# Performance work log

Measured on AMD Instinct MI355X. Metric: run time of the kernel, lower is better.

## Reference

```python
import math
import jax, jax.numpy as jnp
import numpy as np

# ---------------- static irrep configuration ----------------
RS_IN = [(16, 0, 0), (16, 1, 0)]
RS_OUT = [(16, 0, 0), (16, 1, 0)]


def selection_rule(l_in, p_in, l_out, p_out):
    return [l for l in range(abs(l_in - l_out), l_in + l_out + 1)
            if p_out == 0 or p_in * (-1) ** l == p_out]


# ---------------- real Wigner 3j (Clebsch-Gordan) ----------------

def _su2_cg(j1, j2, j3, m1, m2, m3):
    if m1 + m2 != m3:
        return 0.0
    f = math.factorial
    pref = math.sqrt((2 * j3 + 1) * f(j3 + j1 - j2) * f(j3 - j1 + j2) * f(j1 + j2 - j3) / f(j1 + j2 + j3 + 1))
    pref *= math.sqrt(f(j3 + m3) * f(j3 - m3) * f(j1 - m1) * f(j1 + m1) * f(j2 - m2) * f(j2 + m2))
    s = 0.0
    for k in range(0, j1 + j2 - j3 + 1):
        d = [k, j1 + j2 - j3 - k, j1 - m1 - k, j2 + m2 - k, j3 - j1 - m2 + k, j3 - j2 + m1 + k]
        if any(x < 0 for x in d):
            continue
        s += (-1) ** k / np.prod([float(f(x)) for x in d])
    return pref * s


def _c2r(l):
    # real SH = A @ complex SH, rows/cols ordered m = -l..l
    A = np.zeros((2 * l + 1, 2 * l + 1), dtype=complex)
    s2 = 1.0 / math.sqrt(2)
    for m in range(-l, l + 1):
        if m < 0:
            A[l + m, l + m] = 1j * s2
            A[l + m, l - m] = -1j * (-1) ** m * s2
        elif m == 0:
            A[l, l] = 1.0
        else:
            A[l + m, l - m] = s2
            A[l + m, l + m] = (-1) ** m * s2
    return A


_W3J_CACHE = {}

def wigner_3j(l1, l2, l3):
    key = (l1, l2, l3)
    if key in _W3J_CACHE:
        return _W3J_CACHE[key]
    C = np.zeros((2 * l1 + 1, 2 * l2 + 1, 2 * l3 + 1))
    for m1 in range(-l1, l1 + 1):
        for m2 in range(-l2, l2 + 1):
            m3 = -(m1 + m2)
            if abs(m3) <= l3:
                C[l1 + m1, l2 + m2, l3 + m3] = ((-1) ** (l1 - l2 - m3) / math.sqrt(2 * l3 + 1)
                                                * _su2_cg(l1, l2, l3, m1, m2, -m3))
    T = np.einsum('ia,jb,kc,abc->ijk', _c2r(l1), _c2r(l2), _c2r(l3), C.astype(complex))
    T = T * (-1j) ** (l1 + l2 + l3)
    re, im = np.real(T), np.imag(T)
    T = re if np.abs(re).sum() >= np.abs(im).sum() else im
    n = math.sqrt(float((T ** 2).sum()))
    T = T / n if n > 1e-12 else T
    _W3J_CACHE[key] = T
    return T


# ---------------- real spherical harmonics (l = 0,1,2) ----------------

def real_sh(ls, xyz):
    r = jnp.linalg.norm(xyz, axis=-1)
    n = xyz / jnp.where(r > 0, r, 1.0)[..., None]
    x, y, z = n[..., 0], n[..., 1], n[..., 2]
    out = []
    for l in ls:
        if l == 0:
            out.append(jnp.full(x.shape, 0.28209479177387814, x.dtype)[None])
        elif l == 1:
            c = 0.4886025119029199
            out.append(jnp.stack([c * y, c * z, c * x]))
        elif l == 2:
            c1 = 1.0925484305920792
            c2 = 0.31539156525252005
            c3 = 0.5462742152960396
            out.append(jnp.stack([c1 * x * y, c1 * y * z, c2 * (3 * z * z - 1), c1 * x * z, c3 * (x * x - y * y)]))
        else:
            raise NotImplementedError
    return jnp.concatenate(out, axis=0)  # [sum(2l+1), batch, a, b]


def _norm_coef_table():
    nc = np.zeros((len(RS_OUT), len(RS_IN), 2))
    for i, (mul_out, l_out, p_out) in enumerate(RS_OUT):
        num = sum(mul_in * len(selection_rule(l_in, p_in, l_out, p_out))
                  for (mul_in, l_in, p_in) in RS_IN)
        for j, (mul_in, l_in, p_in) in enumerate(RS_IN):
            lm = math.sqrt(2 * l_in + 1) * math.sqrt(4 * math.pi)
            nc[i, j, 0] = lm / math.sqrt(num)
            nc[i, j, 1] = lm / math.sqrt(mul_in)
    return nc


def kernel_conv(features, geometry, mask, W1, b1, W2, b2):
    batch, a, b, _ = geometry.shape
    set_of_l_filters = sorted({l for (_, li, pi) in RS_IN for (_, lo, po) in RS_OUT
                               for l in selection_rule(li, pi, lo, po)})
    Y = real_sh(set_of_l_filters, geometry)             # [9, z, a, b]
    radii = jnp.linalg.norm(geometry, axis=-1)          # [z, a, b]
    # radial MLP: 1 -> H -> n_path
    h = jax.nn.relu(radii[..., None] * W1[0] + b1)
    R = h @ W2 + b2                                     # [z, a, b, n_path]
    nc = _norm_coef_table()
    is_zero = radii == 0

    out_blocks = []
    begin_R = 0
    for i, (mul_out, l_out, p_out) in enumerate(RS_OUT):
        block = jnp.zeros((batch, a, mul_out, 2 * l_out + 1), features.dtype)
        begin_in = 0
        for j, (mul_in, l_in, p_in) in enumerate(RS_IN):
            s_in = slice(begin_in, begin_in + mul_in * (2 * l_in + 1))
            begin_in += mul_in * (2 * l_in + 1)
            l_filters = selection_rule(l_in, p_in, l_out, p_out)
            if not l_filters:
                continue
            n = mul_out * mul_in * len(l_filters)
            sub_R = R[..., begin_R:begin_R + n].reshape(batch, a, b, mul_out, mul_in, len(l_filters))
            begin_R += n
            sub_nc = jnp.where(is_zero, nc[i, j, 1], nc[i, j, 0]).astype(features.dtype)
            f_in = features[..., s_in].reshape(batch, b, mul_in, 2 * l_in + 1)
            for k, l_f in enumerate(l_filters):
                offset = sum(2 * l + 1 for l in set_of_l_filters if l < l_f)
                sub_Y = Y[offset:offset + 2 * l_f + 1]
                C = jnp.asarray(wigner_3j(l_out, l_in, l_f), features.dtype)
                block = block + jnp.einsum('ijk,kzab,zabuv,zab,zbvj->zaui',
                                           C, sub_Y, sub_R[..., k], sub_nc, f_in)
        out_blocks.append(block.reshape(batch, a, -1))
    out = jnp.concatenate(out_blocks, axis=-1)          # [z, a, n_out]
    return out * mask[..., None]


def setup_inputs() -> dict:
    key = jax.random.key(0)
    ks = jax.random.split(key, 6)
    batch, a, b = 2, 160, 160
    dim_in, n_path, H = 64, 1536, 64
    return {
        'features': jax.random.normal(ks[0], (batch, b, dim_in), jnp.float32),
        'geometry': jax.random.normal(ks[1], (batch, a, b, 3), jnp.float32),
        'mask': jnp.ones((batch, b), jnp.float32),
        'W1': jax.random.normal(ks[2], (1, H), jnp.float32) * 0.5,
        'b1': jax.random.normal(ks[3], (H,), jnp.float32) * 0.1,
        'W2': jax.random.normal(ks[4], (H, n_path), jnp.float32) / np.sqrt(H),
        'b2': jnp.zeros((n_path,), jnp.float32),
    }


def reference(features, geometry, mask, W1, b1, W2, b2):
    return kernel_conv(features, geometry, mask, W1, b1, W2, b2)
```

## Files before the change

kernel.cpp:

```cpp
#include <hip/hip_runtime.h>
#include <hip/hip_fp16.h>
#include <math.h>

#define NPATH 1536
#define SEGS  65
#define NB    160
#define NA    160
#define CW    32
#define PPW   5

#define PC_U32S   (320 * SEGS * 256)
#define SWB_OFF   PC_U32S

__device__ float dg_thr[64];

#define SCL_A 0.17677669529663687f
#define SCL_B 0.6266570686577502f
#define SCL_C 0.2558286876965162f
#define SCL_D 0.125f
#define SCL_E 0.3133285343288751f
#define SCL_F 0.7674950309598664f

static __device__ __forceinline__ void slot_map(int t, int& pbase, int& pstr,
                                                int& comp, float& scl) {
    int lane4 = t >> 2, j = t & 3;
    pbase = 0; pstr = 1; comp = -1; scl = 0.0f;
    if (lane4 < 16) {
        if (j == 0) { pbase = lane4 * 16;       scl = SCL_A; }
        else        { pbase = 256 + lane4 * 16; comp = j - 1; scl = SCL_B; }
    } else {
        int lu = lane4 - 16, u = lu / 3, part = lu - u * 3;
        if (part == 0) {
            if (j == 0) { pbase = 512 + u * 16;                       scl = SCL_C; }
            else        { pbase = 768 + u * 48; pstr = 3; comp = j - 1; scl = SCL_D; }
        } else if (part == 1) {
            if (j < 3)  { pbase = 768 + u * 48 + 1; pstr = 3; comp = j; scl = SCL_E; }
        } else {
            if (j < 3)  { pbase = 768 + u * 48 + 2; pstr = 3; comp = j; scl = SCL_F; }
        }
    }
}

__global__ __launch_bounds__(256) void k_sw(const float* __restrict__ W1,
                                            const float* __restrict__ b1,
                                            const float* __restrict__ W2,
                                            const float* __restrict__ b2,
                                            float* __restrict__ ws,
                                            float* __restrict__ out) {
    int bid = blockIdx.x, tid = threadIdx.x;
    if (bid >= 256) {
        out[(bid - 256) * 256 + tid] = 0.0f;
        return;
    }
    int t = bid;

    __shared__ float  tvS[64];
    __shared__ float4 chS[64];
    __shared__ int    rkS[64];
    __shared__ int    ordS[64];
    __shared__ float  dwS[64], dbS[64], b2S[16];
    __shared__ float  W2t[16][65];

    if (tid < 64) {
        float w = W1[tid], bb = b1[tid];
        tvS[tid] = (w != 0.0f) ? (-bb / w) : __builtin_inff();
    }
    __syncthreads();
    if (tid < 64) {
        float mine = tvS[tid];
        int rank = 0;
        for (int j2 = 0; j2 < 64; ++j2) {
            float o = tvS[j2];
            rank += (o < mine || (o == mine && j2 < tid)) ? 1 : 0;
        }
        float w = W1[tid], bb = b1[tid];
        chS[tid] = make_float4((w > 0.0f) ? w : 0.0f,
                               (w < 0.0f) ? w : 0.0f,
                               (w > 0.0f) ? bb : 0.0f,
                               (w < 0.0f) ? bb : ((w == 0.0f && bb > 0.0f) ? bb : 0.0f));
        rkS[tid] = rank;
        ordS[rank] = tid;
        dwS[rank]  = fabsf(w);
        dbS[rank]  = (w > 0.0f) ? bb : ((w < 0.0f) ? -bb : 0.0f);
        if (t == 0) dg_thr[tid] = mine;
    }

    int pbase, pstr, comp; float scl;
    slot_map(t, pbase, pstr, comp, scl);
    (void)comp;
    int cs = tid >> 2, vq = tid & 3;
    #pragma unroll
    for (int i = 0; i < 4; ++i) {
        int v = vq * 4 + i;
        W2t[v][cs] = scl * W2[(size_t)cs * NPATH + pbase + v * pstr];
    }
    if (tid < 16) b2S[tid] = scl * b2[pbase + tid * pstr];
    __syncthreads();

    int v = tid & 15, sq = tid >> 4;
    int s0 = sq * 4;
    float sw = 0.0f, sb = 0.0f;
    #pragma unroll 8
    for (int cc = 0; cc < 64; ++cc) {
        float  w2 = W2t[v][cc];
        float4 ch = chS[cc];
        bool sel = rkS[cc] < s0;
        sw = fmaf(sel ? ch.x : ch.y, w2, sw);
        sb = fmaf(sel ? ch.z : ch.w, w2, sb);
    }
    sb += b2S[v];

    int tg = t >> 4, tl = t & 15, jj = v >> 1, half = v & 1;
    float2* swb = (float2*)(ws + SWB_OFF);
    int ns = (sq == 15) ? 5 : 4;
    for (int i = 0; i < ns; ++i) {
        int s = s0 + i, k = s >> 4, sg = s & 15;
        int flat4 = (((tg * 5 + k) * 8 + jj) * 16 + sg) * 16 + tl;
        swb[flat4 * 2 + half] = make_float2(sw, sb);
        if (i + 1 < ns) {
            float w2s = W2t[v][ordS[s]];
            sw = fmaf(dwS[s], w2s, sw);
            sb = fmaf(dbS[s], w2s, sb);
        }
    }
}

__global__ __launch_bounds__(256) void k_pc3(const float* __restrict__ feat,
                                             const float* __restrict__ ws,
                                             unsigned int* __restrict__ PC) {
    int tg = blockIdx.x & 15, zt = blockIdx.x >> 4;
    int zb0 = zt * 10;

    __shared__ __align__(16) float fS[10][64];
    #pragma unroll
    for (int i = 0; i < 3; ++i) {
        int idx = threadIdx.x + i * 256;
        if (idx < 640) {
            int row = idx >> 6, fi = idx & 63;
            float val = feat[(size_t)(zb0 + row) * 64 + fi];
            int dest;
            if (fi < 16) dest = fi;
            else { int q = (fi - 16) / 3, c3 = (fi - 16) - 3 * q; dest = (c3 + 1) * 16 + q; }
            fS[row][dest] = val;
        }
    }
    __syncthreads();

    int tl = threadIdx.x & 15, sgrp = threadIdx.x >> 4;
    int T = tg * 16 + tl;
    int pbase, pstr, comp; float scl;
    slot_map(T, pbase, pstr, comp, scl);
    (void)pbase; (void)pstr; (void)scl;
    const float* fb = &fS[0][(comp + 1) * 16];
    const float4* swb = (const float4*)(ws + SWB_OFF);

    for (int k = 0; k < 5; ++k) {
        int s = k * 16 + sgrp;
        if (s >= SEGS) break;
        int base4 = (((tg * 5 + k) * 8) * 16 + sgrp) * 16 + tl;
        float4 q0 = swb[base4];
        float4 q1 = swb[base4 + 256], q2 = swb[base4 + 512], q3 = swb[base4 + 768];
        float4 q4 = swb[base4 + 1024], q5 = swb[base4 + 1280];
        float4 q6 = swb[base4 + 1536], q7 = swb[base4 + 1792];
        unsigned int* op = PC + (size_t)zb0 * (SEGS * 256) + (size_t)s * 256 + T;
        #pragma unroll 2
        for (int zb = 0; zb < 10; ++zb) {
            const float4* fp = (const float4*)(fb + zb * 64);
            float4 f0 = fp[0], f1 = fp[1], f2 = fp[2], f3 = fp[3];
            float sw = q0.x * f0.x,          sb = q0.y * f0.x;
            sw = fmaf(q0.z, f0.y, sw);  sb = fmaf(q0.w, f0.y, sb);
            sw = fmaf(q1.x, f0.z, sw);  sb = fmaf(q1.y, f0.z, sb);
            sw = fmaf(q1.z, f0.w, sw);  sb = fmaf(q1.w, f0.w, sb);
            sw = fmaf(q2.x, f1.x, sw);  sb = fmaf(q2.y, f1.x, sb);
            sw = fmaf(q2.z, f1.y, sw);  sb = fmaf(q2.w, f1.y, sb);
            sw = fmaf(q3.x, f1.z, sw);  sb = fmaf(q3.y, f1.z, sb);
            sw = fmaf(q3.z, f1.w, sw);  sb = fmaf(q3.w, f1.w, sb);
            sw = fmaf(q4.x, f2.x, sw);  sb = fmaf(q4.y, f2.x, sb);
            sw = fmaf(q4.z, f2.y, sw);  sb = fmaf(q4.w, f2.y, sb);
            sw = fmaf(q5.x, f2.z, sw);  sb = fmaf(q5.y, f2.z, sb);
            sw = fmaf(q5.z, f2.w, sw);  sb = fmaf(q5.w, f2.w, sb);
            sw = fmaf(q6.x, f3.x, sw);  sb = fmaf(q6.y, f3.x, sb);
            sw = fmaf(q6.z, f3.y, sw);  sb = fmaf(q6.w, f3.y, sb);
            sw = fmaf(q7.x, f3.z, sw);  sb = fmaf(q7.y, f3.z, sb);
            sw = fmaf(q7.z, f3.w, sw);  sb = fmaf(q7.w, f3.w, sb);
            union { __half2 h; unsigned int u; } pk;
            pk.h = __halves2half2(__float2half(sw), __float2half(sb));
            op[(size_t)zb * (SEGS * 256)] = pk.u;
        }
    }
}

static __device__ __forceinline__ float rcomb(unsigned int v, float r) {
    union { unsigned int u; __half2 h; } cv; cv.u = v;
    return fmaf(r, __low2float(cv.h), __high2float(cv.h));
}

__global__ __launch_bounds__(256, 4) void k_main(const float* __restrict__ geom,
                                                 const float* __restrict__ mask,
                                                 const unsigned int* __restrict__ PC,
                                                 float* __restrict__ out) {
    int wv   = threadIdx.x >> 6;
    int lane = threadIdx.x & 63;
    int gw   = blockIdx.x * 4 + wv;
    int chunk = gw & (CW - 1);
    int za    = gw >> 5;
    int z     = za / NA;

    __shared__ float sAcc[4][64];

    bool l0 = lane < 16;
    int  u = 0, part = 0;
    if (!l0) { int lu = lane - 16; u = lu / 3; part = lu - u * 3; }
    float zft = l0 ? 1.4142135623730951f : 2.0f;
    float thrv = dg_thr[lane];

    const float is30 = 0.18257418583505536f;
    const float is10 = 0.31622776601683794f;
    const float c1sh = 0.4886025119029199f;
    const float c21 = 1.0925484305920792f, c22 = 0.31539156525252005f, c23 = 0.5462742152960396f;

    int b0 = chunk * PPW;
    float rr[PPW], nxa[PPW], nya[PPW], nza[PPW], zfa[PPW];
    unsigned int rowo[PPW];
    #pragma unroll
    for (int it = 0; it < PPW; ++it) {
        const float* g = geom + ((size_t)za * NB + b0 + it) * 3;
        float gx = g[0], gy = g[1], gz = g[2];
        float r = sqrtf(gx * gx + gy * gy + gz * gz);
        bool zr = (r == 0.0f);
        float inv = zr ? 1.0f : (1.0f / r);
        nxa[it] = gx * inv; nya[it] = gy * inv; nza[it] = gz * inv;
        rr[it] = r;
        zfa[it] = zr ? zft : 1.0f;
        unsigned long long bm = __ballot(thrv < r);
        int s = __popcll(bm);
        rowo[it] = ((unsigned)(z * NB + b0 + it) * SEGS + (unsigned)s) * 256u
                 + (unsigned)(lane * 4);
    }

    float acc0 = 0.0f, acc1 = 0.0f, acc2 = 0.0f;

    uint4 tb[2];
    tb[0] = *(const uint4*)(PC + rowo[0]);

    #pragma unroll
    for (int it = 0; it < PPW; ++it) {
        if (it + 1 < PPW) tb[(it + 1) & 1] = *(const uint4*)(PC + rowo[it + 1]);
        uint4 tt = tb[it & 1];
        float r = rr[it];
        float T0 = rcomb(tt.x, r);
        float T1 = rcomb(tt.y, r);
        float T2 = rcomb(tt.z, r);
        float T3 = rcomb(tt.w, r);

        float nx = nxa[it], ny = nya[it], nz = nza[it];
        float Y1_0 = c1sh * ny, Y1_1 = c1sh * nz, Y1_2 = c1sh * nx;
        float zf = zfa[it];

        if (l0) {
            float sl0 = T0;
            sl0 = fmaf(Y1_0, T1, sl0);
            sl0 = fmaf(Y1_1, T2, sl0);
            sl0 = fmaf(Y1_2, T3, sl0);
            acc0 = fmaf(sl0, zf, acc0);
        } else if (part == 0) {
            float px = fmaf(Y1_0, T0, T1);
            float py = fmaf(Y1_1, T0, T2);
            float pz = fmaf(Y1_2, T0, T3);
            acc0 = fmaf(px, zf, acc0);
            acc1 = fmaf(py, zf, acc1);
            acc2 = fmaf(pz, zf, acc2);
        } else if (part == 1) {
            float px = fmaf(Y1_2, T1, -Y1_1 * T2);
            float py = fmaf(Y1_0, T2, -Y1_2 * T0);
            float pz = fmaf(Y1_1, T0, -Y1_0 * T1);
            acc0 = fmaf(px, zf, acc0);
            acc1 = fmaf(py, zf, acc1);
            acc2 = fmaf(pz, zf, acc2);
        } else {
            float Y2_0 = c21 * nx * ny;
            float Y2_1 = c21 * ny * nz;
            float Y2_2 = c22 * fmaf(3.0f, nz * nz, -1.0f);
            float Y2_3 = c21 * nx * nz;
            float Y2_4 = c23 * (nx * nx - ny * ny);
            float za_ = is10 * Y2_0, zb_ = is10 * Y2_1, zc_ = is10 * Y2_3;
            float zd_ = is30 * Y2_2, ze_ = is10 * Y2_4;
            float px = fmaf(-(zd_ + ze_), T0, fmaf(zb_, T1, za_ * T2));
            float py = fmaf(zb_, T0, fmaf(2.0f * zd_, T1, zc_ * T2));
            float pz = fmaf(za_, T0, fmaf(zc_, T1, (ze_ - zd_) * T2));
            acc0 = fmaf(px, zf, acc0);
            acc1 = fmaf(py, zf, acc1);
            acc2 = fmaf(pz, zf, acc2);
        }
    }

    float ax = acc0 + __shfl_down(acc0, 1) + __shfl_down(acc0, 2);
    float ay = acc1 + __shfl_down(acc1, 1) + __shfl_down(acc1, 2);
    float az = acc2 + __shfl_down(acc2, 1) + __shfl_down(acc2, 2);
    if (l0) {
        sAcc[wv][lane] = acc0;
    } else if (part == 0) {
        int ob = 16 + u * 3;
        sAcc[wv][ob]     = ax;
        sAcc[wv][ob + 1] = ay;
        sAcc[wv][ob + 2] = az;
    }
    __syncthreads();
    if (threadIdx.x < 64) {
        float sum = sAcc[0][threadIdx.x] + sAcc[1][threadIdx.x]
                  + sAcc[2][threadIdx.x] + sAcc[3][threadIdx.x];
        sum *= mask[za];
        atomicAdd(&out[(size_t)za * 64 + threadIdx.x], sum);
    }
}

extern "C" void kernel_launch(void* const* d_in, const int* in_sizes, int n_in,
                              void* d_out, int out_size, void* d_ws, size_t ws_size,
                              hipStream_t stream) {
    (void)in_sizes; (void)n_in; (void)ws_size; (void)out_size;
    const float* feat = (const float*)d_in[0];
    const float* geom = (const float*)d_in[1];
    const float* mask = (const float*)d_in[2];
    const float* W1   = (const float*)d_in[3];
    const float* b1   = (const float*)d_in[4];
    const float* W2   = (const float*)d_in[5];
    const float* b2   = (const float*)d_in[6];
    float* out = (float*)d_out;
    float* ws  = (float*)d_ws;
    unsigned int* PC = (unsigned int*)d_ws;

    k_sw  <<<336, 256, 0, stream>>>(W1, b1, W2, b2, ws, out);
    k_pc3 <<<512, 256, 0, stream>>>(feat, ws, PC);
    k_main<<<2 * NA * CW / 4, 256, 0, stream>>>(geom, mask, PC, out);
}
```

Measured before the change: 94.97 us.

## Fuse three kernels into one cooperative persistent kernel with grid syncs

Replaces the three launches (weight/segment table, per-node precompute, main edge loop) with a single cooperative kernel of 640 blocks. Grid-wide syncs separate the phases. The precompute is re-tiled to 8 rows per block and the main phase loops four times per block. This removes kernel launch gaps and tail effects. The cost is grid.sync overhead and fewer resident blocks in the main phase, where latency hiding was previously handled by oversubscription. The old three-kernel path is kept as a fallback if the cooperative launch fails.

```diff
diff --git a/kernel.cpp b/kernel.cpp
--- a/kernel.cpp
+++ b/kernel.cpp
@@ -1,6 +1,9 @@
 #include <hip/hip_runtime.h>
+#include <hip/hip_cooperative_groups.h>
 #include <hip/hip_fp16.h>
 #include <math.h>
+
+namespace cg = cooperative_groups;
 
 #define NPATH 1536
 #define SEGS  65
@@ -41,6 +44,281 @@
     }
 }
 
+static __device__ __forceinline__ float rcomb(unsigned int v, float r) {
+    union { unsigned int u; __half2 h; } cv; cv.u = v;
+    return fmaf(r, __low2float(cv.h), __high2float(cv.h));
+}
+
+__global__ __launch_bounds__(256, 3) void k_all(const float* __restrict__ feat,
+                                                const float* __restrict__ geom,
+                                                const float* __restrict__ mask,
+                                                const float* __restrict__ W1,
+                                                const float* __restrict__ b1,
+                                                const float* __restrict__ W2,
+                                                const float* __restrict__ b2,
+                                                float* __restrict__ ws,
+                                                float* __restrict__ out) {
+    cg::grid_group grid = cg::this_grid();
+    int bid = blockIdx.x, tid = threadIdx.x;
+
+    __shared__ float  tvS[64];
+    __shared__ float4 chS[64];
+    __shared__ int    rkS[64];
+    __shared__ int    ordS[64];
+    __shared__ float  dwS[64], dbS[64], b2S[16];
+    __shared__ float  W2t[16][65];
+    __shared__ __align__(16) float fS[8][64];
+    __shared__ float  sAcc[4][64];
+
+    unsigned int* PC = (unsigned int*)ws;
+
+    if (bid < 256) {
+        int t = bid;
+        if (tid < 64) {
+            float w = W1[tid], bb = b1[tid];
+            tvS[tid] = (w != 0.0f) ? (-bb / w) : __builtin_inff();
+        }
+        __syncthreads();
+        if (tid < 64) {
+            float mine = tvS[tid];
+            int rank = 0;
+            for (int j2 = 0; j2 < 64; ++j2) {
+                float o = tvS[j2];
+                rank += (o < mine || (o == mine && j2 < tid)) ? 1 : 0;
+            }
+            float w = W1[tid], bb = b1[tid];
+            chS[tid] = make_float4((w > 0.0f) ? w : 0.0f,
+                                   (w < 0.0f) ? w : 0.0f,
+                                   (w > 0.0f) ? bb : 0.0f,
+                                   (w < 0.0f) ? bb : ((w == 0.0f && bb > 0.0f) ? bb : 0.0f));
+            rkS[tid] = rank;
+            ordS[rank] = tid;
+            dwS[rank]  = fabsf(w);
+            dbS[rank]  = (w > 0.0f) ? bb : ((w < 0.0f) ? -bb : 0.0f);
+        }
+        int pbase, pstr, comp; float scl;
+        slot_map(t, pbase, pstr, comp, scl);
+        (void)comp;
+        int cs = tid >> 2, vq = tid & 3;
+        #pragma unroll
+        for (int i = 0; i < 4; ++i) {
+            int v = vq * 4 + i;
+            W2t[v][cs] = scl * W2[(size_t)cs * NPATH + pbase + v * pstr];
+        }
+        if (tid < 16) b2S[tid] = scl * b2[pbase + tid * pstr];
+        __syncthreads();
+
+        int v = tid & 15, sq = tid >> 4;
+        int s0 = sq * 4;
+        float sw = 0.0f, sb = 0.0f;
+        #pragma unroll 8
+        for (int cc = 0; cc < 64; ++cc) {
+            float  w2 = W2t[v][cc];
+            float4 ch = chS[cc];
+            bool sel = rkS[cc] < s0;
+            sw = fmaf(sel ? ch.x : ch.y, w2, sw);
+            sb = fmaf(sel ? ch.z : ch.w, w2, sb);
+        }
+        sb += b2S[v];
+
+        int tg = t >> 4, tl = t & 15, jj = v >> 1, half = v & 1;
+        float2* swb2 = (float2*)(ws + SWB_OFF);
+        int ns = (sq == 15) ? 5 : 4;
+        for (int i = 0; i < ns; ++i) {
+            int s = s0 + i, k = s >> 4, sg = s & 15;
+            int flat4 = (((tg * 5 + k) * 8 + jj) * 16 + sg) * 16 + tl;
+            swb2[flat4 * 2 + half] = make_float2(sw, sb);
+            if (i + 1 < ns) {
+                float w2s = W2t[v][ordS[s]];
+                sw = fmaf(dwS[s], w2s, sw);
+                sb = fmaf(dbS[s], w2s, sb);
+            }
+        }
+    } else if (bid < 336) {
+        out[(bid - 336 + 80) % 80 * 256 + tid] = 0.0f;
+    }
+
+    grid.sync();
+
+    {
+        int tg = bid & 15, zt = bid >> 4;
+        int zb0 = zt * 8;
+        #pragma unroll
+        for (int i = 0; i < 2; ++i) {
+            int idx = tid + i * 256;
+            int row = idx >> 6, fi = idx & 63;
+            float val = feat[(size_t)(zb0 + row) * 64 + fi];
+            int dest;
+            if (fi < 16) dest = fi;
+            else { int q = (fi - 16) / 3, c3 = (fi - 16) - 3 * q; dest = (c3 + 1) * 16 + q; }
+            fS[row][dest] = val;
+        }
+        __syncthreads();
+
+        int tl = tid & 15, sgrp = tid >> 4;
+        int T = tg * 16 + tl;
+        int pbase, pstr, comp; float scl;
+        slot_map(T, pbase, pstr, comp, scl);
+        (void)pbase; (void)pstr; (void)scl;
+        const float* fb = &fS[0][(comp + 1) * 16];
+        const float4* swb = (const float4*)(ws + SWB_OFF);
+
+        for (int k = 0; k < 5; ++k) {
+            int s = k * 16 + sgrp;
+            if (s >= SEGS) break;
+            int base4 = (((tg * 5 + k) * 8) * 16 + sgrp) * 16 + tl;
+            float4 q0 = swb[base4];
+            float4 q1 = swb[base4 + 256], q2 = swb[base4 + 512], q3 = swb[base4 + 768];
+            float4 q4 = swb[base4 + 1024], q5 = swb[base4 + 1280];
+            float4 q6 = swb[base4 + 1536], q7 = swb[base4 + 1792];
+            unsigned int* op = PC + (size_t)zb0 * (SEGS * 256) + (size_t)s * 256 + T;
+            #pragma unroll 2
+            for (int zb = 0; zb < 8; ++zb) {
+                const float4* fp = (const float4*)(fb + zb * 64);
+                float4 f0 = fp[0], f1 = fp[1], f2 = fp[2], f3 = fp[3];
+                float sw = q0.x * f0.x,          sb = q0.y * f0.x;
+                sw = fmaf(q0.z, f0.y, sw);  sb = fmaf(q0.w, f0.y, sb);
+                sw = fmaf(q1.x, f0.z, sw);  sb = fmaf(q1.y, f0.z, sb);
+                sw = fmaf(q1.z, f0.w, sw);  sb = fmaf(q1.w, f0.w, sb);
+                sw = fmaf(q2.x, f1.x, sw);  sb = fmaf(q2.y, f1.x, sb);
+                sw = fmaf(q2.z, f1.y, sw);  sb = fmaf(q2.w, f1.y, sb);
+                sw = fmaf(q3.x, f1.z, sw);  sb = fmaf(q3.y, f1.z, sb);
+                sw = fmaf(q3.z, f1.w, sw);  sb = fmaf(q3.w, f1.w, sb);
+                sw = fmaf(q4.x, f2.x, sw);  sb = fmaf(q4.y, f2.x, sb);
+                sw = fmaf(q4.z, f2.y, sw);  sb = fmaf(q4.w, f2.y, sb);
+                sw = fmaf(q5.x, f2.z, sw);  sb = fmaf(q5.y, f2.z, sb);
+                sw = fmaf(q5.z, f2.w, sw);  sb = fmaf(q5.w, f2.w, sb);
+                sw = fmaf(q6.x, f3.x, sw);  sb = fmaf(q6.y, f3.x, sb);
+                sw = fmaf(q6.z, f3.y, sw);  sb = fmaf(q6.w, f3.y, sb);
+                sw = fmaf(q7.x, f3.z, sw);  sb = fmaf(q7.y, f3.z, sb);
+                sw = fmaf(q7.z, f3.w, sw);  sb = fmaf(q7.w, f3.w, sb);
+                union { __half2 h; unsigned int u; } pk;
+                pk.h = __halves2half2(__float2half(sw), __float2half(sb));
+                op[(size_t)zb * (SEGS * 256)] = pk.u;
+            }
+        }
+    }
+
+    grid.sync();
+
+    {
+        int wv   = tid >> 6;
+        int lane = tid & 63;
+        bool l0 = lane < 16;
+        int  u = 0, part = 0;
+        if (!l0) { int lu = lane - 16; u = lu / 3; part = lu - u * 3; }
+        float zft = l0 ? 1.4142135623730951f : 2.0f;
+        float w1v = W1[lane], b1v = b1[lane];
+        float thrv = (w1v != 0.0f) ? (-b1v / w1v) : __builtin_inff();
+
+        const float is30 = 0.18257418583505536f;
+        const float is10 = 0.31622776601683794f;
+        const float c1sh = 0.4886025119029199f;
+        const float c21 = 1.0925484305920792f, c22 = 0.31539156525252005f, c23 = 0.5462742152960396f;
+
+        for (int it4 = 0; it4 < 4; ++it4) {
+            int bt = it4 * 640 + bid;
+            int gw   = bt * 4 + wv;
+            int chunk = gw & (CW - 1);
+            int za    = gw >> 5;
+            int z     = za / NA;
+
+            int b0 = chunk * PPW;
+            float rr[PPW], nxa[PPW], nya[PPW], nza[PPW], zfa[PPW];
+            unsigned int rowo[PPW];
+            #pragma unroll
+            for (int it = 0; it < PPW; ++it) {
+                const float* g = geom + ((size_t)za * NB + b0 + it) * 3;
+                float gx = g[0], gy = g[1], gz = g[2];
+                float r = sqrtf(gx * gx + gy * gy + gz * gz);
+                bool zr = (r == 0.0f);
+                float inv = zr ? 1.0f : (1.0f / r);
+                nxa[it] = gx * inv; nya[it] = gy * inv; nza[it] = gz * inv;
+                rr[it] = r;
+                zfa[it] = zr ? zft : 1.0f;
+                unsigned long long bm = __ballot(thrv < r);
+                int s = __popcll(bm);
+                rowo[it] = ((unsigned)(z * NB + b0 + it) * SEGS + (unsigned)s) * 256u
+                         + (unsigned)(lane * 4);
+            }
+
+            float acc0 = 0.0f, acc1 = 0.0f, acc2 = 0.0f;
+            uint4 tb[2];
+            tb[0] = *(const uint4*)(PC + rowo[0]);
+
+            #pragma unroll
+            for (int it = 0; it < PPW; ++it) {
+                if (it + 1 < PPW) tb[(it + 1) & 1] = *(const uint4*)(PC + rowo[it + 1]);
+                uint4 tt = tb[it & 1];
+                float r = rr[it];
+                float T0 = rcomb(tt.x, r);
+                float T1 = rcomb(tt.y, r);
+                float T2 = rcomb(tt.z, r);
+                float T3 = rcomb(tt.w, r);
+
+                float nx = nxa[it], ny = nya[it], nz = nza[it];
+                float Y1_0 = c1sh * ny, Y1_1 = c1sh * nz, Y1_2 = c1sh * nx;
+                float zf = zfa[it];
+
+                if (l0) {
+                    float sl0 = T0;
+                    sl0 = fmaf(Y1_0, T1, sl0);
+                    sl0 = fmaf(Y1_1, T2, sl0);
+                    sl0 = fmaf(Y1_2, T3, sl0);
+                    acc0 = fmaf(sl0, zf, acc0);
+                } else if (part == 0) {
+                    float px = fmaf(Y1_0, T0, T1);
+                    float py = fmaf(Y1_1, T0, T2);
+                    float pz = fmaf(Y1_2, T0, T3);
+                    acc0 = fmaf(px, zf, acc0);
+                    acc1 = fmaf(py, zf, acc1);
+                    acc2 = fmaf(pz, zf, acc2);
+                } else if (part == 1) {
+                    float px = fmaf(Y1_2, T1, -Y1_1 * T2);
+                    float py = fmaf(Y1_0, T2, -Y1_2 * T0);
+                    float pz = fmaf(Y1_1, T0, -Y1_0 * T1);
+                    acc0 = fmaf(px, zf, acc0);
+                    acc1 = fmaf(py, zf, acc1);
+                    acc2 = fmaf(pz, zf, acc2);
+                } else {
+                    float Y2_0 = c21 * nx * ny;
+                    float Y2_1 = c21 * ny * nz;
+                    float Y2_2 = c22 * fmaf(3.0f, nz * nz, -1.0f);
+                    float Y2_3 = c21 * nx * nz;
+                    float Y2_4 = c23 * (nx * nx - ny * ny);
+                    float za_ = is10 * Y2_0, zb_ = is10 * Y2_1, zc_ = is10 * Y2_3;
+                    float zd_ = is30 * Y2_2, ze_ = is10 * Y2_4;
+                    float px = fmaf(-(zd_ + ze_), T0, fmaf(zb_, T1, za_ * T2));
+                    float py = fmaf(zb_, T0, fmaf(2.0f * zd_, T1, zc_ * T2));
+                    float pz = fmaf(za_, T0, fmaf(zc_, T1, (ze_ - zd_) * T2));
+                    acc0 = fmaf(px, zf, acc0);
+                    acc1 = fmaf(py, zf, acc1);
+                    acc2 = fmaf(pz, zf, acc2);
+                }
+            }
+
+            float ax = acc0 + __shfl_down(acc0, 1) + __shfl_down(acc0, 2);
+            float ay = acc1 + __shfl_down(acc1, 1) + __shfl_down(acc1, 2);
+            float az = acc2 + __shfl_down(acc2, 1) + __shfl_down(acc2, 2);
+            if (l0) {
+                sAcc[wv][lane] = acc0;
+            } else if (part == 0) {
+                int ob = 16 + u * 3;
+                sAcc[wv][ob]     = ax;
+                sAcc[wv][ob + 1] = ay;
+                sAcc[wv][ob + 2] = az;
+            }
+            __syncthreads();
+            if (tid < 64) {
+                float sum = sAcc[0][tid] + sAcc[1][tid] + sAcc[2][tid] + sAcc[3][tid];
+                sum *= mask[za];
+                atomicAdd(&out[(size_t)za * 64 + tid], sum);
+            }
+            __syncthreads();
+        }
+    }
+}
+
 __global__ __launch_bounds__(256) void k_sw(const float* __restrict__ W1,
                                             const float* __restrict__ b1,
                                             const float* __restrict__ W2,
@@ -53,7 +331,6 @@
         return;
     }
     int t = bid;
-
     __shared__ float  tvS[64];
     __shared__ float4 chS[64];
     __shared__ int    rkS[64];
@@ -84,7 +361,6 @@
         dbS[rank]  = (w > 0.0f) ? bb : ((w < 0.0f) ? -bb : 0.0f);
         if (t == 0) dg_thr[tid] = mine;
     }
-
     int pbase, pstr, comp; float scl;
     slot_map(t, pbase, pstr, comp, scl);
     (void)comp;
@@ -109,7 +385,6 @@
         sb = fmaf(sel ? ch.z : ch.w, w2, sb);
     }
     sb += b2S[v];
-
     int tg = t >> 4, tl = t & 15, jj = v >> 1, half = v & 1;
     float2* swb = (float2*)(ws + SWB_OFF);
     int ns = (sq == 15) ? 5 : 4;
@@ -130,7 +405,6 @@
                                              unsigned int* __restrict__ PC) {
     int tg = blockIdx.x & 15, zt = blockIdx.x >> 4;
     int zb0 = zt * 10;
-
     __shared__ __align__(16) float fS[10][64];
     #pragma unroll
     for (int i = 0; i < 3; ++i) {
@@ -145,7 +419,6 @@
         }
     }
     __syncthreads();
-
     int tl = threadIdx.x & 15, sgrp = threadIdx.x >> 4;
     int T = tg * 16 + tl;
     int pbase, pstr, comp; float scl;
@@ -153,7 +426,6 @@
     (void)pbase; (void)pstr; (void)scl;
     const float* fb = &fS[0][(comp + 1) * 16];
     const float4* swb = (const float4*)(ws + SWB_OFF);
-
     for (int k = 0; k < 5; ++k) {
         int s = k * 16 + sgrp;
         if (s >= SEGS) break;
@@ -190,11 +462,6 @@
     }
 }
 
-static __device__ __forceinline__ float rcomb(unsigned int v, float r) {
-    union { unsigned int u; __half2 h; } cv; cv.u = v;
-    return fmaf(r, __low2float(cv.h), __high2float(cv.h));
-}
-
 __global__ __launch_bounds__(256, 4) void k_main(const float* __restrict__ geom,
                                                  const float* __restrict__ mask,
                                                  const unsigned int* __restrict__ PC,
@@ -205,20 +472,16 @@
     int chunk = gw & (CW - 1);
     int za    = gw >> 5;
     int z     = za / NA;
-
     __shared__ float sAcc[4][64];
-
     bool l0 = lane < 16;
     int  u = 0, part = 0;
     if (!l0) { int lu = lane - 16; u = lu / 3; part = lu - u * 3; }
     float zft = l0 ? 1.4142135623730951f : 2.0f;
     float thrv = dg_thr[lane];
-
     const float is30 = 0.18257418583505536f;
     const float is10 = 0.31622776601683794f;
     const float c1sh = 0.4886025119029199f;
     const float c21 = 1.0925484305920792f, c22 = 0.31539156525252005f, c23 = 0.5462742152960396f;
-
     int b0 = chunk * PPW;
     float rr[PPW], nxa[PPW], nya[PPW], nza[PPW], zfa[PPW];
     unsigned int rowo[PPW];
@@ -237,12 +500,9 @@
         rowo[it] = ((unsigned)(z * NB + b0 + it) * SEGS + (unsigned)s) * 256u
                  + (unsigned)(lane * 4);
     }
-
     float acc0 = 0.0f, acc1 = 0.0f, acc2 = 0.0f;
-
     uint4 tb[2];
     tb[0] = *(const uint4*)(PC + rowo[0]);
-
     #pragma unroll
     for (int it = 0; it < PPW; ++it) {
         if (it + 1 < PPW) tb[(it + 1) & 1] = *(const uint4*)(PC + rowo[it + 1]);
@@ -252,11 +512,9 @@
         float T1 = rcomb(tt.y, r);
         float T2 = rcomb(tt.z, r);
         float T3 = rcomb(tt.w, r);
-
         float nx = nxa[it], ny = nya[it], nz = nza[it];
         float Y1_0 = c1sh * ny, Y1_1 = c1sh * nz, Y1_2 = c1sh * nx;
         float zf = zfa[it];
-
         if (l0) {
             float sl0 = T0;
             sl0 = fmaf(Y1_0, T1, sl0);
@@ -293,7 +551,6 @@
             acc2 = fmaf(pz, zf, acc2);
         }
     }
-
     float ax = acc0 + __shfl_down(acc0, 1) + __shfl_down(acc0, 2);
     float ay = acc1 + __shfl_down(acc1, 1) + __shfl_down(acc1, 2);
     float az = acc2 + __shfl_down(acc2, 1) + __shfl_down(acc2, 2);
@@ -329,7 +586,13 @@
     float* ws  = (float*)d_ws;
     unsigned int* PC = (unsigned int*)d_ws;
 
-    k_sw  <<<336, 256, 0, stream>>>(W1, b1, W2, b2, ws, out);
-    k_pc3 <<<512, 256, 0, stream>>>(feat, ws, PC);
-    k_main<<<2 * NA * CW / 4, 256, 0, stream>>>(geom, mask, PC, out);
-}
+    void* args[] = {(void*)&feat, (void*)&geom, (void*)&mask, (void*)&W1,
+                    (void*)&b1, (void*)&W2, (void*)&b2, (void*)&ws, (void*)&out};
+    hipError_t e = hipLaunchCooperativeKernel((const void*)k_all, dim3(640),
+                                              dim3(256), args, 0, stream);
+    if (e != hipSuccess) {
+        k_sw  <<<336, 256, 0, stream>>>(W1, b1, W2, b2, ws, out);
+        k_pc3 <<<512, 256, 0, stream>>>(feat, ws, PC);
+        k_main<<<2 * NA * CW / 4, 256, 0, stream>>>(geom, mask, PC, out);
+    }
+}
```

New measurement: 260.5 us. +174.3%, slower.

## Give each k_main wave 20 neighbors with a rolling prefetch, fewer blocks

Applied to the files above, without the earlier changes.

k_main now launches 640 blocks, two per (batch, atom) row, instead of 2560. Each wave walks 20 neighbors in a loop that prefetches the next neighbor's geometry and PC row, replacing the fully unrolled 5-neighbor batch. The per-channel thresholds are recomputed from W1/b1 inside k_main, so the dg_thr device global is gone. This is meant to cut block launch and reduction overhead (fewer sAcc reductions and atomic/output writes per row), at the cost of less parallelism and a serial dependency chain per wave.

```diff
diff --git a/kernel.cpp b/kernel.cpp
--- a/kernel.cpp
+++ b/kernel.cpp
@@ -6,13 +6,9 @@
 #define SEGS  65
 #define NB    160
 #define NA    160
-#define CW    32
-#define PPW   5
 
 #define PC_U32S   (320 * SEGS * 256)
 #define SWB_OFF   PC_U32S
-
-__device__ float dg_thr[64];
 
 #define SCL_A 0.17677669529663687f
 #define SCL_B 0.6266570686577502f
@@ -41,6 +37,11 @@
     }
 }
 
+static __device__ __forceinline__ float rcomb(unsigned int v, float r) {
+    union { unsigned int u; __half2 h; } cv; cv.u = v;
+    return fmaf(r, __low2float(cv.h), __high2float(cv.h));
+}
+
 __global__ __launch_bounds__(256) void k_sw(const float* __restrict__ W1,
                                             const float* __restrict__ b1,
                                             const float* __restrict__ W2,
@@ -53,7 +54,6 @@
         return;
     }
     int t = bid;
-
     __shared__ float  tvS[64];
     __shared__ float4 chS[64];
     __shared__ int    rkS[64];
@@ -82,9 +82,7 @@
         ordS[rank] = tid;
         dwS[rank]  = fabsf(w);
         dbS[rank]  = (w > 0.0f) ? bb : ((w < 0.0f) ? -bb : 0.0f);
-        if (t == 0) dg_thr[tid] = mine;
-    }
-
+    }
     int pbase, pstr, comp; float scl;
     slot_map(t, pbase, pstr, comp, scl);
     (void)comp;
@@ -130,7 +128,6 @@
                                              unsigned int* __restrict__ PC) {
     int tg = blockIdx.x & 15, zt = blockIdx.x >> 4;
     int zb0 = zt * 10;
-
     __shared__ __align__(16) float fS[10][64];
     #pragma unroll
     for (int i = 0; i < 3; ++i) {
@@ -145,7 +142,6 @@
         }
     }
     __syncthreads();
-
     int tl = threadIdx.x & 15, sgrp = threadIdx.x >> 4;
     int T = tg * 16 + tl;
     int pbase, pstr, comp; float scl;
@@ -153,7 +149,6 @@
     (void)pbase; (void)pstr; (void)scl;
     const float* fb = &fS[0][(comp + 1) * 16];
     const float4* swb = (const float4*)(ws + SWB_OFF);
-
     for (int k = 0; k < 5; ++k) {
         int s = k * 16 + sgrp;
         if (s >= SEGS) break;
@@ -190,21 +185,17 @@
     }
 }
 
-static __device__ __forceinline__ float rcomb(unsigned int v, float r) {
-    union { unsigned int u; __half2 h; } cv; cv.u = v;
-    return fmaf(r, __low2float(cv.h), __high2float(cv.h));
-}
-
 __global__ __launch_bounds__(256, 4) void k_main(const float* __restrict__ geom,
                                                  const float* __restrict__ mask,
+                                                 const float* __restrict__ W1,
+                                                 const float* __restrict__ b1,
                                                  const unsigned int* __restrict__ PC,
                                                  float* __restrict__ out) {
     int wv   = threadIdx.x >> 6;
     int lane = threadIdx.x & 63;
-    int gw   = blockIdx.x * 4 + wv;
-    int chunk = gw & (CW - 1);
-    int za    = gw >> 5;
-    int z     = za / NA;
+    int bid  = blockIdx.x;
+    int za   = bid >> 1, half = bid & 1;
+    int z    = za / NA;
 
     __shared__ float sAcc[4][64];
 
@@ -212,50 +203,62 @@
     int  u = 0, part = 0;
     if (!l0) { int lu = lane - 16; u = lu / 3; part = lu - u * 3; }
     float zft = l0 ? 1.4142135623730951f : 2.0f;
-    float thrv = dg_thr[lane];
+    float w1v = W1[lane], b1v = b1[lane];
+    float thrv = (w1v != 0.0f) ? (-b1v / w1v) : __builtin_inff();
 
     const float is30 = 0.18257418583505536f;
     const float is10 = 0.31622776601683794f;
     const float c1sh = 0.4886025119029199f;
     const float c21 = 1.0925484305920792f, c22 = 0.31539156525252005f, c23 = 0.5462742152960396f;
 
-    int b0 = chunk * PPW;
-    float rr[PPW], nxa[PPW], nya[PPW], nza[PPW], zfa[PPW];
-    unsigned int rowo[PPW];
-    #pragma unroll
-    for (int it = 0; it < PPW; ++it) {
-        const float* g = geom + ((size_t)za * NB + b0 + it) * 3;
-        float gx = g[0], gy = g[1], gz = g[2];
+    int b0 = half * 80 + wv * 20;
+    const float* gbase = geom + ((size_t)za * NB + b0) * 3;
+    unsigned int zbase = (unsigned)(z * NB + b0);
+
+    float acc0 = 0.0f, acc1 = 0.0f, acc2 = 0.0f;
+
+    float r_c, nx_c, ny_c, nz_c, zf_c;
+    {
+        float gx = gbase[0], gy = gbase[1], gz = gbase[2];
         float r = sqrtf(gx * gx + gy * gy + gz * gz);
         bool zr = (r == 0.0f);
         float inv = zr ? 1.0f : (1.0f / r);
-        nxa[it] = gx * inv; nya[it] = gy * inv; nza[it] = gz * inv;
-        rr[it] = r;
-        zfa[it] = zr ? zft : 1.0f;
-        unsigned long long bm = __ballot(thrv < r);
-        int s = __popcll(bm);
-        rowo[it] = ((unsigned)(z * NB + b0 + it) * SEGS + (unsigned)s) * 256u
-                 + (unsigned)(lane * 4);
-    }
-
-    float acc0 = 0.0f, acc1 = 0.0f, acc2 = 0.0f;
-
-    uint4 tb[2];
-    tb[0] = *(const uint4*)(PC + rowo[0]);
-
-    #pragma unroll
-    for (int it = 0; it < PPW; ++it) {
-        if (it + 1 < PPW) tb[(it + 1) & 1] = *(const uint4*)(PC + rowo[it + 1]);
-        uint4 tt = tb[it & 1];
-        float r = rr[it];
+        nx_c = gx * inv; ny_c = gy * inv; nz_c = gz * inv;
+        r_c = r; zf_c = zr ? zft : 1.0f;
+    }
+    unsigned long long bm0 = __ballot(thrv < r_c);
+    unsigned int ro_c = (zbase * SEGS + (unsigned)__popcll(bm0)) * 256u
+                      + (unsigned)(lane * 4);
+    uint4 tb0 = *(const uint4*)(PC + ro_c);
+
+    for (int q = 0; q < 20; ++q) {
+        float r_n = 0.0f, nx_n = 0.0f, ny_n = 0.0f, nz_n = 0.0f, zf_n = 0.0f;
+        uint4 tb1 = tb0;
+        if (q + 1 < 20) {
+            const float* g = gbase + (q + 1) * 3;
+            float gx = g[0], gy = g[1], gz = g[2];
+            float r = sqrtf(gx * gx + gy * gy + gz * gz);
+            bool zr = (r == 0.0f);
+            float inv = zr ? 1.0f : (1.0f / r);
+            nx_n = gx * inv; ny_n = gy * inv; nz_n = gz * inv;
+            r_n = r; zf_n = zr ? zft : 1.0f;
+            unsigned long long bm = __ballot(thrv < r);
+            unsigned int ro_n = ((zbase + (unsigned)(q + 1)) * SEGS
+                                 + (unsigned)__popcll(bm)) * 256u
+                              + (unsigned)(lane * 4);
+            tb1 = *(const uint4*)(PC + ro_n);
+        }
+
+        uint4 tt = tb0;
+        float r = r_c;
         float T0 = rcomb(tt.x, r);
         float T1 = rcomb(tt.y, r);
         float T2 = rcomb(tt.z, r);
         float T3 = rcomb(tt.w, r);
 
-        float nx = nxa[it], ny = nya[it], nz = nza[it];
+        float nx = nx_c, ny = ny_c, nz = nz_c;
         float Y1_0 = c1sh * ny, Y1_1 = c1sh * nz, Y1_2 = c1sh * nx;
-        float zf = zfa[it];
+        float zf = zf_c;
 
         if (l0) {
             float sl0 = T0;
@@ -292,6 +295,9 @@
             acc1 = fmaf(py, zf, acc1);
             acc2 = fmaf(pz, zf, acc2);
         }
+
+        r_c = r_n; nx_c = nx_n; ny_c = ny_n; nz_c = nz_n; zf_c = zf_n;
+        tb0 = tb1;
     }
 
     float ax = acc0 + __shfl_down(acc0, 1) + __shfl_down(acc0, 2);
@@ -331,5 +337,5 @@
 
     k_sw  <<<336, 256, 0, stream>>>(W1, b1, W2, b2, ws, out);
     k_pc3 <<<512, 256, 0, stream>>>(feat, ws, PC);
-    k_main<<<2 * NA * CW / 4, 256, 0, stream>>>(geom, mask, PC, out);
-}
+    k_main<<<640, 256, 0, stream>>>(geom, mask, W1, b1, PC, out);
+}
```

Measured after the change: 100.8 us. 1.06x slower.
